# Optimization experiments

Hardware: AMD Instinct MI355X
Metric: run time of the kernel (lower is better)

Reference implementation:

```python
import jax, jax.numpy as jnp
import numpy as np

N, E, D_IN, D_OUT, K = 50000, 800000, 128, 128, 3

def setup_inputs() -> dict:
    key = jax.random.key(0)
    k1, k2, k3, k4, k5 = jax.random.split(key, 5)
    feat = jax.random.normal(k1, (N, D_IN), dtype=jnp.float32)
    src = jax.random.randint(k2, (E,), 0, N)
    dst = jax.random.randint(k3, (E,), 0, N)
    theta = 0.1 * jax.random.normal(k4, (K + 1,), dtype=jnp.float32)
    # xavier-uniform-like linear weight [out, in]
    lim = float(np.sqrt(6.0 / (D_IN + D_OUT)))
    W = jax.random.uniform(k5, (D_OUT, D_IN), minval=-lim, maxval=lim, dtype=jnp.float32)
    return {"feat": feat, "src": src, "dst": dst, "theta": theta, "W": W}

def reference(feat, src, dst, theta, W):
    n = feat.shape[0]
    # in-degree per destination node, clamped to >= 1
    deg = jax.ops.segment_sum(jnp.ones_like(dst, dtype=feat.dtype), dst, num_segments=n)
    d_invsqrt = jnp.maximum(deg, 1.0) ** -0.5  # [N]
    d_invsqrt = d_invsqrt[:, None]

    def L_prime(x):
        # -D^{-1/2} A D^{-1/2} x  (A aggregates src -> dst)
        msg = (x * d_invsqrt)[src]                      # [E, D]
        agg = jax.ops.segment_sum(msg, dst, num_segments=n)
        return -agg * d_invsqrt

    k = theta.shape[0] - 1
    h = theta[0] * feat
    T_km2 = feat
    T_km1 = L_prime(feat)
    if k >= 1:
        h = h + theta[1] * (T_km1 + 1.0) * 0.5
    for order in range(2, k + 1):
        T_k = 2.0 * L_prime(T_km1) - T_km2
        h = h + theta[order] * (T_k + 1.0) * 0.5
        T_km2, T_km1 = T_km1, T_k

    out = h @ W.T  # linear, no bias
    return jax.nn.leaky_relu(out, negative_slope=0.01)
```

## Files before the change

kernel.cpp:

```cpp
#include <hip/hip_runtime.h>

#define NN 50000
#define EE 800000
#define D 128
#define PARTSZ 6250

static inline size_t align_up(size_t x, size_t a) { return (x + a - 1) & ~(a - 1); }

__device__ __forceinline__ unsigned pack_bf16(float a, float b) {
    unsigned ua = __float_as_uint(a), ub = __float_as_uint(b);
    unsigned ra = (ua + 0x7fffu + ((ua >> 16) & 1u)) >> 16;
    unsigned rb = (ub + 0x7fffu + ((ub >> 16) & 1u)) & 0xffff0000u;
    return ra | rb;
}
__device__ __forceinline__ float bf_lo(unsigned u) { return __uint_as_float(u << 16); }
__device__ __forceinline__ float bf_hi(unsigned u) { return __uint_as_float(u & 0xffff0000u); }

__global__ __launch_bounds__(256) void deg_kernel(const int* __restrict__ dst,
                                                  int* __restrict__ deg, int E) {
    int part = blockIdx.x & 7;
    int nch = gridDim.x >> 3;
    int chunk = blockIdx.x >> 3;
    int per = (E + nch - 1) / nch;
    int beg = chunk * per;
    int end = min(E, beg + per);
    int plo = part * PARTSZ, phi = plo + PARTSZ;
    for (int e = beg + threadIdx.x; e < end; e += 256) {
        int d = dst[e];
        if (d >= plo && d < phi) atomicAdd(&deg[d], 1);
    }
}

__global__ void dinv_kernel(const int* __restrict__ deg, float* __restrict__ dinv, int n) {
    int i = blockIdx.x * blockDim.x + threadIdx.x;
    if (i < n) {
        float d = (float)deg[i];
        dinv[i] = rsqrtf(d > 1.0f ? d : 1.0f);
    }
}

__global__ void scale_kernel(const float* __restrict__ feat, const float* __restrict__ dinv,
                             unsigned* __restrict__ featb, int n) {
    int idx = blockIdx.x * blockDim.x + threadIdx.x;
    if (idx >= n * 64) return;
    int i = idx >> 6;
    float di = dinv[i];
    float2 f = ((const float2*)feat)[idx];
    featb[idx] = pack_bf16(f.x * di, f.y * di);
}

__global__ void scan_blk_kernel(const int* __restrict__ deg, int* __restrict__ bscan,
                                int* __restrict__ btot, int n) {
    __shared__ int ws4[4];
    int tid = threadIdx.x, b = blockIdx.x;
    int i = b * 256 + tid;
    int v = (i < n) ? deg[i] : 0;
    int lane = tid & 63, w = tid >> 6;
    int sc = v;
    #pragma unroll
    for (int off = 1; off < 64; off <<= 1) {
        int t = __shfl_up(sc, off);
        if (lane >= off) sc += t;
    }
    if (lane == 63) ws4[w] = sc;
    __syncthreads();
    int woff = 0;
    #pragma unroll
    for (int k = 0; k < 4; ++k)
        if (k < w) woff += ws4[k];
    int inc = sc + woff;
    bscan[b * 256 + tid] = inc;
    if (tid == 255) btot[b] = inc;
}

__global__ void scan_top_kernel(int* __restrict__ btot, int nb) {
    __shared__ int ws4[4];
    int tid = threadIdx.x;
    int v = (tid < nb) ? btot[tid] : 0;
    int lane = tid & 63, w = tid >> 6;
    int sc = v;
    #pragma unroll
    for (int off = 1; off < 64; off <<= 1) {
        int t = __shfl_up(sc, off);
        if (lane >= off) sc += t;
    }
    if (lane == 63) ws4[w] = sc;
    __syncthreads();
    int woff = 0;
    #pragma unroll
    for (int k = 0; k < 4; ++k)
        if (k < w) woff += ws4[k];
    if (tid < nb) btot[tid] = sc + woff - v;
}

__global__ void scan_fix_kernel(const int* __restrict__ bscan, const int* __restrict__ btot,
                                const int* __restrict__ deg, int* __restrict__ rowptr,
                                int* __restrict__ cursor, int n) {
    int i = blockIdx.x * blockDim.x + threadIdx.x;
    if (i >= n) return;
    int inc = bscan[i] + btot[i >> 8];
    rowptr[i + 1] = inc;
    cursor[i] = inc - deg[i];
    if (i == 0) rowptr[0] = 0;
}

__global__ __launch_bounds__(256) void scatter_kernel(const int* __restrict__ src,
                                                      const int* __restrict__ dst,
                                                      int* __restrict__ cursor,
                                                      int* __restrict__ csr_src, int E) {
    int part = blockIdx.x & 7;
    int nch = gridDim.x >> 3;
    int chunk = blockIdx.x >> 3;
    int per = (E + nch - 1) / nch;
    int beg = chunk * per;
    int end = min(E, beg + per);
    int plo = part * PARTSZ, phi = plo + PARTSZ;
    for (int e = beg + threadIdx.x; e < end; e += 256) {
        int d = dst[e];
        int s = src[e];
        if (d >= plo && d < phi) {
            int p = atomicAdd(&cursor[d], 1);
            csr_src[p] = s;
        }
    }
}

template <int MODE>
__global__ __launch_bounds__(256) void agg_kernel(
    const int* __restrict__ rowptr, const int* __restrict__ csr_src,
    const float* __restrict__ dinv, const unsigned* __restrict__ Xb,
    const float* __restrict__ feat, const float* __restrict__ T1f,
    const float* __restrict__ T2f, const float* __restrict__ theta,
    float* __restrict__ outf, unsigned* __restrict__ outb, int n) {
    int wid = (blockIdx.x * blockDim.x + threadIdx.x) >> 6;
    int lane = threadIdx.x & 63;
    if (wid >= n) return;
    int half = lane >> 5;
    int hl = lane & 31;
    int beg = rowptr[wid];
    int end = rowptr[wid + 1];
    const uint2* X2 = (const uint2*)Xb;
    float a0 = 0.f, a1 = 0.f, a2 = 0.f, a3 = 0.f;
    for (int e0 = beg; e0 < end; e0 += 64) {
        int s = (e0 + lane < end) ? csr_src[e0 + lane] : 0;
        int cnt = min(64, end - e0);
        int j = 0;
        for (; j + 8 <= cnt; j += 8) {
            int s0 = __shfl(s, j + 0 + half);
            int s1 = __shfl(s, j + 2 + half);
            int s2 = __shfl(s, j + 4 + half);
            int s3 = __shfl(s, j + 6 + half);
            uint2 u0 = X2[(size_t)s0 * 32 + hl];
            uint2 u1 = X2[(size_t)s1 * 32 + hl];
            uint2 u2 = X2[(size_t)s2 * 32 + hl];
            uint2 u3 = X2[(size_t)s3 * 32 + hl];
            a0 += bf_lo(u0.x); a1 += bf_hi(u0.x); a2 += bf_lo(u0.y); a3 += bf_hi(u0.y);
            a0 += bf_lo(u1.x); a1 += bf_hi(u1.x); a2 += bf_lo(u1.y); a3 += bf_hi(u1.y);
            a0 += bf_lo(u2.x); a1 += bf_hi(u2.x); a2 += bf_lo(u2.y); a3 += bf_hi(u2.y);
            a0 += bf_lo(u3.x); a1 += bf_hi(u3.x); a2 += bf_lo(u3.y); a3 += bf_hi(u3.y);
        }
        for (; j + 2 <= cnt; j += 2) {
            int sj = __shfl(s, j + half);
            uint2 u = X2[(size_t)sj * 32 + hl];
            a0 += bf_lo(u.x); a1 += bf_hi(u.x); a2 += bf_lo(u.y); a3 += bf_hi(u.y);
        }
        if (j < cnt) {
            int sj = __shfl(s, j);
            if (half == 0) {
                uint2 u = X2[(size_t)sj * 32 + hl];
                a0 += bf_lo(u.x); a1 += bf_hi(u.x); a2 += bf_lo(u.y); a3 += bf_hi(u.y);
            }
        }
    }
    a0 += __shfl_xor(a0, 32);
    a1 += __shfl_xor(a1, 32);
    a2 += __shfl_xor(a2, 32);
    a3 += __shfl_xor(a3, 32);

    float di = dinv[wid];
    size_t row4 = (size_t)wid * 32 + hl;
    float r0, r1, r2, r3;
    if (MODE == 1) {
        r0 = -di * a0; r1 = -di * a1; r2 = -di * a2; r3 = -di * a3;
    } else if (MODE == 2) {
        float4 f = ((const float4*)feat)[row4];
        r0 = -2.f * di * a0 - f.x;
        r1 = -2.f * di * a1 - f.y;
        r2 = -2.f * di * a2 - f.z;
        r3 = -2.f * di * a3 - f.w;
    } else {
        float4 f = ((const float4*)feat)[row4];
        float4 t1 = ((const float4*)T1f)[row4];
        float4 t2 = ((const float4*)T2f)[row4];
        float th0 = theta[0], th1 = theta[1], th2 = theta[2], th3 = theta[3];
        float c = 0.5f * (th1 + th2 + th3);
        float t30 = -2.f * di * a0 - t1.x;
        float t31 = -2.f * di * a1 - t1.y;
        float t32 = -2.f * di * a2 - t1.z;
        float t33 = -2.f * di * a3 - t1.w;
        r0 = th0 * f.x + 0.5f * (th1 * t1.x + th2 * t2.x + th3 * t30) + c;
        r1 = th0 * f.y + 0.5f * (th1 * t1.y + th2 * t2.y + th3 * t31) + c;
        r2 = th0 * f.z + 0.5f * (th1 * t1.z + th2 * t2.z + th3 * t32) + c;
        r3 = th0 * f.w + 0.5f * (th1 * t1.w + th2 * t2.w + th3 * t33) + c;
    }
    if (half == 0) {
        ((float4*)outf)[row4] = make_float4(r0, r1, r2, r3);
    } else if (MODE != 3) {
        uint2 p;
        p.x = pack_bf16(r0 * di, r1 * di);
        p.y = pack_bf16(r2 * di, r3 * di);
        ((uint2*)outb)[row4] = p;
    }
}

#define BK 32
#define TS 68
__global__ __launch_bounds__(256) void gemm_kernel(const float* __restrict__ h,
                                                   const float* __restrict__ W,
                                                   float* __restrict__ out, int n) {
    __shared__ float hs[BK * TS];
    __shared__ float ws[BK * TS];
    int tid = threadIdx.x;
    int tile = blockIdx.x >> 1;
    int o0 = (blockIdx.x & 1) * 64;
    int node0 = tile * 64;
    int tx = tid & 15, ty = tid >> 4;

    float acc[4][4] = {};

    for (int k0 = 0; k0 < D; k0 += BK) {
        __syncthreads();
        #pragma unroll
        for (int p = 0; p < 2; ++p) {
            int idx = p * 256 + tid;
            int r = idx >> 3, c4 = idx & 7;
            int nn = node0 + r;
            float4 v = make_float4(0.f, 0.f, 0.f, 0.f);
            if (nn < n) v = ((const float4*)(h + (size_t)nn * D + k0))[c4];
            hs[(c4 * 4 + 0) * TS + r] = v.x;
            hs[(c4 * 4 + 1) * TS + r] = v.y;
            hs[(c4 * 4 + 2) * TS + r] = v.z;
            hs[(c4 * 4 + 3) * TS + r] = v.w;
            float4 wv = ((const float4*)(W + (size_t)(o0 + r) * D + k0))[c4];
            ws[(c4 * 4 + 0) * TS + r] = wv.x;
            ws[(c4 * 4 + 1) * TS + r] = wv.y;
            ws[(c4 * 4 + 2) * TS + r] = wv.z;
            ws[(c4 * 4 + 3) * TS + r] = wv.w;
        }
        __syncthreads();
        #pragma unroll
        for (int kk = 0; kk < BK; ++kk) {
            float4 hv = *(const float4*)&hs[kk * TS + 4 * ty];
            float4 wv = *(const float4*)&ws[kk * TS + 4 * tx];
            float hvv[4] = {hv.x, hv.y, hv.z, hv.w};
            float wvv[4] = {wv.x, wv.y, wv.z, wv.w};
            #pragma unroll
            for (int k = 0; k < 4; ++k)
                #pragma unroll
                for (int kk2 = 0; kk2 < 4; ++kk2)
                    acc[k][kk2] = fmaf(hvv[k], wvv[kk2], acc[k][kk2]);
        }
    }

    #pragma unroll
    for (int k = 0; k < 4; ++k) {
        int nn = node0 + 4 * ty + k;
        if (nn < n) {
            float4 r4;
            r4.x = acc[k][0] > 0.f ? acc[k][0] : 0.01f * acc[k][0];
            r4.y = acc[k][1] > 0.f ? acc[k][1] : 0.01f * acc[k][1];
            r4.z = acc[k][2] > 0.f ? acc[k][2] : 0.01f * acc[k][2];
            r4.w = acc[k][3] > 0.f ? acc[k][3] : 0.01f * acc[k][3];
            ((float4*)(out + (size_t)nn * D + o0))[tx] = r4;
        }
    }
}

extern "C" void kernel_launch(void* const* d_in, const int* in_sizes, int n_in,
                              void* d_out, int out_size, void* d_ws, size_t ws_size,
                              hipStream_t stream) {
    const float* feat = (const float*)d_in[0];
    const int* src = (const int*)d_in[1];
    const int* dst = (const int*)d_in[2];
    const float* theta = (const float*)d_in[3];
    const float* W = (const float*)d_in[4];
    float* out = (float*)d_out;

    const int n = NN;
    const int E = EE;
    const int nb = (n + 255) / 256;

    char* w = (char*)d_ws;
    size_t off = 0;
    int* deg = (int*)(w + off); off = align_up(off + (size_t)n * 4, 512);
    float* dinv = (float*)(w + off); off = align_up(off + (size_t)n * 4, 512);
    int* rowptr = (int*)(w + off); off = align_up(off + (size_t)(n + 1) * 4, 512);
    int* cursor = (int*)(w + off); off = align_up(off + (size_t)n * 4, 512);
    int* bscan = (int*)(w + off); off = align_up(off + (size_t)(nb * 256) * 4, 512);
    int* btot = (int*)(w + off); off = align_up(off + (size_t)256 * 4, 512);
    int* csr_src = (int*)(w + off); off = align_up(off + (size_t)E * 4, 512);
    unsigned* featb = (unsigned*)(w + off); off = align_up(off + (size_t)n * 64 * 4, 512);
    float* T1f = (float*)(w + off); off = align_up(off + (size_t)n * D * 4, 512);
    unsigned* T1b = (unsigned*)(w + off); off = align_up(off + (size_t)n * 64 * 4, 512);
    float* T2f = (float*)(w + off); off = align_up(off + (size_t)n * D * 4, 512);
    unsigned* T2b = (unsigned*)(w + off); off = align_up(off + (size_t)n * 64 * 4, 512);
    (void)ws_size;

    hipMemsetAsync(deg, 0, (size_t)n * 4, stream);

    deg_kernel<<<2048, 256, 0, stream>>>(dst, deg, E);
    dinv_kernel<<<(n + 255) / 256, 256, 0, stream>>>(deg, dinv, n);
    scale_kernel<<<(n * 64 + 255) / 256, 256, 0, stream>>>(feat, dinv, featb, n);
    scan_blk_kernel<<<nb, 256, 0, stream>>>(deg, bscan, btot, n);
    scan_top_kernel<<<1, 256, 0, stream>>>(btot, nb);
    scan_fix_kernel<<<(n + 255) / 256, 256, 0, stream>>>(bscan, btot, deg, rowptr, cursor, n);
    scatter_kernel<<<2048, 256, 0, stream>>>(src, dst, cursor, csr_src, E);

    int agg_grid = (n + 3) / 4;
    agg_kernel<1><<<agg_grid, 256, 0, stream>>>(rowptr, csr_src, dinv, featb, feat, T1f, T2f, theta, T1f, T1b, n);
    agg_kernel<2><<<agg_grid, 256, 0, stream>>>(rowptr, csr_src, dinv, T1b, feat, T1f, T2f, theta, T2f, T2b, n);
    agg_kernel<3><<<agg_grid, 256, 0, stream>>>(rowptr, csr_src, dinv, T2b, feat, T1f, T2f, theta, T1f, (unsigned*)0, n);

    int gemm_grid = ((n + 63) / 64) * 2;
    gemm_kernel<<<gemm_grid, 256, 0, stream>>>(T1f, W, out, n);
}
```

Measured before the change: 238.5 us.

## Keep Chebyshev intermediates and h only in bf16, dropping fp32 copies

After: 227.7 us. -4.6%, faster.

```diff
diff --git a/kernel.cpp b/kernel.cpp
--- a/kernel.cpp
+++ b/kernel.cpp
@@ -15,6 +15,11 @@
 }
 __device__ __forceinline__ float bf_lo(unsigned u) { return __uint_as_float(u << 16); }
 __device__ __forceinline__ float bf_hi(unsigned u) { return __uint_as_float(u & 0xffff0000u); }
+
+__global__ void zero_kernel(int* __restrict__ p, int n) {
+    int i = blockIdx.x * blockDim.x + threadIdx.x;
+    if (i < n) p[i] = 0;
+}
 
 __global__ __launch_bounds__(256) void deg_kernel(const int* __restrict__ dst,
                                                   int* __restrict__ deg, int E) {
@@ -31,11 +36,14 @@
     }
 }
 
-__global__ void dinv_kernel(const int* __restrict__ deg, float* __restrict__ dinv, int n) {
+__global__ void dinv_kernel(const int* __restrict__ deg, float* __restrict__ dinv,
+                            float* __restrict__ rdinv, int n) {
     int i = blockIdx.x * blockDim.x + threadIdx.x;
     if (i < n) {
         float d = (float)deg[i];
-        dinv[i] = rsqrtf(d > 1.0f ? d : 1.0f);
+        if (d < 1.0f) d = 1.0f;
+        dinv[i] = rsqrtf(d);
+        rdinv[i] = sqrtf(d);
     }
 }
 
@@ -128,10 +136,10 @@
 template <int MODE>
 __global__ __launch_bounds__(256) void agg_kernel(
     const int* __restrict__ rowptr, const int* __restrict__ csr_src,
-    const float* __restrict__ dinv, const unsigned* __restrict__ Xb,
-    const float* __restrict__ feat, const float* __restrict__ T1f,
-    const float* __restrict__ T2f, const float* __restrict__ theta,
-    float* __restrict__ outf, unsigned* __restrict__ outb, int n) {
+    const float* __restrict__ dinv, const float* __restrict__ rdinv,
+    const unsigned* __restrict__ Xb, const float* __restrict__ feat,
+    const unsigned* __restrict__ T1b, const float* __restrict__ theta,
+    unsigned* __restrict__ outb, int n) {
     int wid = (blockIdx.x * blockDim.x + threadIdx.x) >> 6;
     int lane = threadIdx.x & 63;
     if (wid >= n) return;
@@ -179,43 +187,57 @@
 
     float di = dinv[wid];
     size_t row4 = (size_t)wid * 32 + hl;
-    float r0, r1, r2, r3;
     if (MODE == 1) {
-        r0 = -di * a0; r1 = -di * a1; r2 = -di * a2; r3 = -di * a3;
+        if (half == 0) {
+            float r0 = -di * a0, r1 = -di * a1, r2 = -di * a2, r3 = -di * a3;
+            uint2 p;
+            p.x = pack_bf16(r0 * di, r1 * di);
+            p.y = pack_bf16(r2 * di, r3 * di);
+            ((uint2*)outb)[row4] = p;
+        }
     } else if (MODE == 2) {
-        float4 f = ((const float4*)feat)[row4];
-        r0 = -2.f * di * a0 - f.x;
-        r1 = -2.f * di * a1 - f.y;
-        r2 = -2.f * di * a2 - f.z;
-        r3 = -2.f * di * a3 - f.w;
+        if (half == 0) {
+            float4 f = ((const float4*)feat)[row4];
+            float r0 = -2.f * di * a0 - f.x;
+            float r1 = -2.f * di * a1 - f.y;
+            float r2 = -2.f * di * a2 - f.z;
+            float r3 = -2.f * di * a3 - f.w;
+            uint2 p;
+            p.x = pack_bf16(r0 * di, r1 * di);
+            p.y = pack_bf16(r2 * di, r3 * di);
+            ((uint2*)outb)[row4] = p;
+        }
     } else {
-        float4 f = ((const float4*)feat)[row4];
-        float4 t1 = ((const float4*)T1f)[row4];
-        float4 t2 = ((const float4*)T2f)[row4];
-        float th0 = theta[0], th1 = theta[1], th2 = theta[2], th3 = theta[3];
-        float c = 0.5f * (th1 + th2 + th3);
-        float t30 = -2.f * di * a0 - t1.x;
-        float t31 = -2.f * di * a1 - t1.y;
-        float t32 = -2.f * di * a2 - t1.z;
-        float t33 = -2.f * di * a3 - t1.w;
-        r0 = th0 * f.x + 0.5f * (th1 * t1.x + th2 * t2.x + th3 * t30) + c;
-        r1 = th0 * f.y + 0.5f * (th1 * t1.y + th2 * t2.y + th3 * t31) + c;
-        r2 = th0 * f.z + 0.5f * (th1 * t1.z + th2 * t2.z + th3 * t32) + c;
-        r3 = th0 * f.w + 0.5f * (th1 * t1.w + th2 * t2.w + th3 * t33) + c;
-    }
-    if (half == 0) {
-        ((float4*)outf)[row4] = make_float4(r0, r1, r2, r3);
-    } else if (MODE != 3) {
-        uint2 p;
-        p.x = pack_bf16(r0 * di, r1 * di);
-        p.y = pack_bf16(r2 * di, r3 * di);
-        ((uint2*)outb)[row4] = p;
+        if (half == 0) {
+            float rd = rdinv[wid];
+            float4 f = ((const float4*)feat)[row4];
+            uint2 ub1 = ((const uint2*)T1b)[row4];
+            uint2 ub2 = ((const uint2*)Xb)[row4];
+            float t10 = bf_lo(ub1.x) * rd, t11 = bf_hi(ub1.x) * rd;
+            float t12 = bf_lo(ub1.y) * rd, t13 = bf_hi(ub1.y) * rd;
+            float t20 = bf_lo(ub2.x) * rd, t21 = bf_hi(ub2.x) * rd;
+            float t22 = bf_lo(ub2.y) * rd, t23 = bf_hi(ub2.y) * rd;
+            float th0 = theta[0], th1 = theta[1], th2 = theta[2], th3 = theta[3];
+            float c = 0.5f * (th1 + th2 + th3);
+            float t30 = -2.f * di * a0 - t10;
+            float t31 = -2.f * di * a1 - t11;
+            float t32 = -2.f * di * a2 - t12;
+            float t33 = -2.f * di * a3 - t13;
+            float r0 = th0 * f.x + 0.5f * (th1 * t10 + th2 * t20 + th3 * t30) + c;
+            float r1 = th0 * f.y + 0.5f * (th1 * t11 + th2 * t21 + th3 * t31) + c;
+            float r2 = th0 * f.z + 0.5f * (th1 * t12 + th2 * t22 + th3 * t32) + c;
+            float r3 = th0 * f.w + 0.5f * (th1 * t13 + th2 * t23 + th3 * t33) + c;
+            uint2 p;
+            p.x = pack_bf16(r0, r1);
+            p.y = pack_bf16(r2, r3);
+            ((uint2*)outb)[row4] = p;
+        }
     }
 }
 
 #define BK 32
 #define TS 68
-__global__ __launch_bounds__(256) void gemm_kernel(const float* __restrict__ h,
+__global__ __launch_bounds__(256) void gemm_kernel(const unsigned* __restrict__ hb,
                                                    const float* __restrict__ W,
                                                    float* __restrict__ out, int n) {
     __shared__ float hs[BK * TS];
@@ -225,6 +247,7 @@
     int o0 = (blockIdx.x & 1) * 64;
     int node0 = tile * 64;
     int tx = tid & 15, ty = tid >> 4;
+    const uint2* H2 = (const uint2*)hb;
 
     float acc[4][4] = {};
 
@@ -233,19 +256,19 @@
         #pragma unroll
         for (int p = 0; p < 2; ++p) {
             int idx = p * 256 + tid;
-            int r = idx >> 3, c4 = idx & 7;
+            int r = idx >> 3, c = idx & 7;
             int nn = node0 + r;
-            float4 v = make_float4(0.f, 0.f, 0.f, 0.f);
-            if (nn < n) v = ((const float4*)(h + (size_t)nn * D + k0))[c4];
-            hs[(c4 * 4 + 0) * TS + r] = v.x;
-            hs[(c4 * 4 + 1) * TS + r] = v.y;
-            hs[(c4 * 4 + 2) * TS + r] = v.z;
-            hs[(c4 * 4 + 3) * TS + r] = v.w;
-            float4 wv = ((const float4*)(W + (size_t)(o0 + r) * D + k0))[c4];
-            ws[(c4 * 4 + 0) * TS + r] = wv.x;
-            ws[(c4 * 4 + 1) * TS + r] = wv.y;
-            ws[(c4 * 4 + 2) * TS + r] = wv.z;
-            ws[(c4 * 4 + 3) * TS + r] = wv.w;
+            uint2 u = make_uint2(0u, 0u);
+            if (nn < n) u = H2[(size_t)nn * 32 + (k0 >> 2) + c];
+            hs[(c * 4 + 0) * TS + r] = bf_lo(u.x);
+            hs[(c * 4 + 1) * TS + r] = bf_hi(u.x);
+            hs[(c * 4 + 2) * TS + r] = bf_lo(u.y);
+            hs[(c * 4 + 3) * TS + r] = bf_hi(u.y);
+            float4 wv = ((const float4*)(W + (size_t)(o0 + r) * D + k0))[c];
+            ws[(c * 4 + 0) * TS + r] = wv.x;
+            ws[(c * 4 + 1) * TS + r] = wv.y;
+            ws[(c * 4 + 2) * TS + r] = wv.z;
+            ws[(c * 4 + 3) * TS + r] = wv.w;
         }
         __syncthreads();
         #pragma unroll
@@ -294,22 +317,21 @@
     size_t off = 0;
     int* deg = (int*)(w + off); off = align_up(off + (size_t)n * 4, 512);
     float* dinv = (float*)(w + off); off = align_up(off + (size_t)n * 4, 512);
+    float* rdinv = (float*)(w + off); off = align_up(off + (size_t)n * 4, 512);
     int* rowptr = (int*)(w + off); off = align_up(off + (size_t)(n + 1) * 4, 512);
     int* cursor = (int*)(w + off); off = align_up(off + (size_t)n * 4, 512);
     int* bscan = (int*)(w + off); off = align_up(off + (size_t)(nb * 256) * 4, 512);
     int* btot = (int*)(w + off); off = align_up(off + (size_t)256 * 4, 512);
     int* csr_src = (int*)(w + off); off = align_up(off + (size_t)E * 4, 512);
     unsigned* featb = (unsigned*)(w + off); off = align_up(off + (size_t)n * 64 * 4, 512);
-    float* T1f = (float*)(w + off); off = align_up(off + (size_t)n * D * 4, 512);
     unsigned* T1b = (unsigned*)(w + off); off = align_up(off + (size_t)n * 64 * 4, 512);
-    float* T2f = (float*)(w + off); off = align_up(off + (size_t)n * D * 4, 512);
     unsigned* T2b = (unsigned*)(w + off); off = align_up(off + (size_t)n * 64 * 4, 512);
+    unsigned* hb = (unsigned*)(w + off); off = align_up(off + (size_t)n * 64 * 4, 512);
     (void)ws_size;
 
-    hipMemsetAsync(deg, 0, (size_t)n * 4, stream);
-
+    zero_kernel<<<(n + 255) / 256, 256, 0, stream>>>(deg, n);
     deg_kernel<<<2048, 256, 0, stream>>>(dst, deg, E);
-    dinv_kernel<<<(n + 255) / 256, 256, 0, stream>>>(deg, dinv, n);
+    dinv_kernel<<<(n + 255) / 256, 256, 0, stream>>>(deg, dinv, rdinv, n);
     scale_kernel<<<(n * 64 + 255) / 256, 256, 0, stream>>>(feat, dinv, featb, n);
     scan_blk_kernel<<<nb, 256, 0, stream>>>(deg, bscan, btot, n);
     scan_top_kernel<<<1, 256, 0, stream>>>(btot, nb);
@@ -317,10 +339,10 @@
     scatter_kernel<<<2048, 256, 0, stream>>>(src, dst, cursor, csr_src, E);
 
     int agg_grid = (n + 3) / 4;
-    agg_kernel<1><<<agg_grid, 256, 0, stream>>>(rowptr, csr_src, dinv, featb, feat, T1f, T2f, theta, T1f, T1b, n);
-    agg_kernel<2><<<agg_grid, 256, 0, stream>>>(rowptr, csr_src, dinv, T1b, feat, T1f, T2f, theta, T2f, T2b, n);
-    agg_kernel<3><<<agg_grid, 256, 0, stream>>>(rowptr, csr_src, dinv, T2b, feat, T1f, T2f, theta, T1f, (unsigned*)0, n);
+    agg_kernel<1><<<agg_grid, 256, 0, stream>>>(rowptr, csr_src, dinv, rdinv, featb, feat, T1b, theta, T1b, n);
+    agg_kernel<2><<<agg_grid, 256, 0, stream>>>(rowptr, csr_src, dinv, rdinv, T1b, feat, T1b, theta, T2b, n);
+    agg_kernel<3><<<agg_grid, 256, 0, stream>>>(rowptr, csr_src, dinv, rdinv, T2b, feat, T1b, theta, hb, n);
 
     int gemm_grid = ((n + 63) / 64) * 2;
-    gemm_kernel<<<gemm_grid, 256, 0, stream>>>(T1f, W, out, n);
-}
+    gemm_kernel<<<gemm_grid, 256, 0, stream>>>(hb, W, out, n);
+}
```
